# Kernel optimization log

Hardware: AMD Instinct MI355X
Metric: run time of the kernel (lower is better)

## Reference

```python
import jax, jax.numpy as jnp
import numpy as np

N_NODES = 50000
D_MODEL = 128
N_EDGES = 600000
HIDDEN = 128
EDGE_FEAT = 2 * D_MODEL + 2  # 258


def setup_inputs() -> dict:
    key = jax.random.key(0)
    k = jax.random.split(key, 8)
    H = jax.random.normal(k[0], (N_NODES, D_MODEL), dtype=jnp.float32)
    edge_index = jax.random.randint(k[1], (2, N_EDGES), 0, N_NODES, dtype=jnp.int64)
    S_e = jax.random.uniform(k[2], (N_EDGES,), dtype=jnp.float32)
    F_e = jax.random.uniform(k[3], (N_EDGES,), dtype=jnp.float32)
    W1 = jax.random.normal(k[4], (EDGE_FEAT, HIDDEN), dtype=jnp.float32) * (1.0 / np.sqrt(EDGE_FEAT))
    b1 = jnp.zeros((HIDDEN,), dtype=jnp.float32)
    W2 = jax.random.normal(k[5], (HIDDEN, 1), dtype=jnp.float32) * (1.0 / np.sqrt(HIDDEN))
    b2 = jnp.zeros((1,), dtype=jnp.float32)
    return {"H": H, "edge_index": edge_index, "S_e": S_e, "F_e": F_e,
            "W1": W1, "b1": b1, "W2": W2, "b2": b2}


def reference(H, edge_index, S_e, F_e, W1, b1, W2, b2):
    # Gather endpoint node features: [E, D]
    H_u = H[edge_index[0]]
    H_v = H[edge_index[1]]
    H_diff = jnp.abs(H_u - H_v)
    H_prod = H_u * H_v
    # [E, 2D+2]
    edge_features = jnp.concatenate(
        [H_diff, H_prod, S_e[:, None], F_e[:, None]], axis=1)
    # 2-layer MLP with SiLU (dropout is identity in eval mode)
    h = jax.nn.silu(edge_features @ W1 + b1)
    a_e = (h @ W2 + b2)[:, 0]  # [E]
    return a_e
```

## Files before the change

kernel.cpp:

```cpp
#include <hip/hip_runtime.h>


typedef _Float16       half8   __attribute__((ext_vector_type(8)));
typedef _Float16       half4v  __attribute__((ext_vector_type(4)));
typedef unsigned short ushort8 __attribute__((ext_vector_type(8)));
typedef float          f32x4   __attribute__((ext_vector_type(4)));

#define NSEG    8

__device__ __forceinline__ float silu_f(float x) {
    return x / (1.0f + __expf(-x));
}


__global__ __launch_bounds__(256)
void cvt_h_kernel(const float* __restrict__ H, _Float16* __restrict__ Hh, int n4) {
    int i = blockIdx.x * blockDim.x + threadIdx.x;
    if (i < n4) {
        const float4 f = ((const float4*)H)[i];
        half4v h;
        h[0] = (_Float16)f.x; h[1] = (_Float16)f.y;
        h[2] = (_Float16)f.z; h[3] = (_Float16)f.w;
        ((half4v*)Hh)[i] = h;
    }
}

__device__ __forceinline__ void canon(int u, int v, int& a, int& b) {
    const int sw = (u ^ v) & 1;
    a = sw ? v : u;
    b = sw ? u : v;
}

__global__ __launch_bounds__(256)
void hist_kernel(const int* __restrict__ eidx, int* __restrict__ hist,
                 int E, int ASZ, int BBINS) {
    int e = blockIdx.x * blockDim.x + threadIdx.x;
    if (e < E) {
        int a, b;
        canon(eidx[e], eidx[E + e], a, b);
        atomicAdd(&hist[(a / ASZ) * BBINS + (b >> 3)], 1);
    }
}

__global__ __launch_bounds__(256)
void scan1_kernel(int* __restrict__ hist, int* __restrict__ bsum, int NB) {
    __shared__ int s[256];
    const int t = threadIdx.x;
    const int i = blockIdx.x * 256 + t;
    const int v = (i < NB) ? hist[i] : 0;
    s[t] = v;
    __syncthreads();
    for (int off = 1; off < 256; off <<= 1) {
        const int x = (t >= off) ? s[t - off] : 0;
        __syncthreads();
        s[t] += x;
        __syncthreads();
    }
    if (i < NB) hist[i] = s[t] - v;
    if (t == 255) bsum[blockIdx.x] = s[255];
}

__global__ __launch_bounds__(256)
void scan2_kernel(int* __restrict__ bsum, int nb1) {
    __shared__ int s[256];
    const int t = threadIdx.x;
    const int v = (t < nb1) ? bsum[t] : 0;
    s[t] = v;
    __syncthreads();
    for (int off = 1; off < 256; off <<= 1) {
        const int x = (t >= off) ? s[t - off] : 0;
        __syncthreads();
        s[t] += x;
        __syncthreads();
    }
    if (t < nb1) bsum[t] = s[t] - v;
}

__global__ __launch_bounds__(256)
void scan3_kernel(int* __restrict__ hist, const int* __restrict__ bsum, int NB) {
    const int i = blockIdx.x * 256 + threadIdx.x;
    if (i < NB) hist[i] += bsum[blockIdx.x];
}

__global__ __launch_bounds__(64)
void segb_kernel(const int* __restrict__ hist, int* __restrict__ vbs,
                 int BBINS, int E) {
    const int t = threadIdx.x;
    if (t < NSEG) vbs[t] = hist[t * BBINS];
    else if (t == NSEG) vbs[NSEG] = E;
}

__global__ __launch_bounds__(256)
void scatter_kernel(const int* __restrict__ eidx, const float* __restrict__ Se,
                    const float* __restrict__ Fe, int* __restrict__ ofs,
                    int4* __restrict__ recs, int E, int ASZ, int BBINS) {
    int e = blockIdx.x * blockDim.x + threadIdx.x;
    if (e < E) {
        int a, b;
        canon(eidx[e], eidx[E + e], a, b);
        const int key = (a / ASZ) * BBINS + (b >> 3);
        const int pos = atomicAdd(&ofs[key], 1);
        _Float16 sh = (_Float16)Se[e];
        _Float16 fh = (_Float16)Fe[e];
        unsigned pk = (unsigned)*(unsigned short*)&sh
                    | ((unsigned)*(unsigned short*)&fh << 16);
        recs[pos] = make_int4(a, b, e, (int)pk);
    }
}


__device__ __forceinline__ void stage_w1(const float* __restrict__ W1,
                                         _Float16* __restrict__ w1t, int tid) {
    const int n = tid & 127;
    const int g = tid >> 7;
    #pragma unroll
    for (int i = 0; i < 8; ++i) {
        const int kb = g + (i << 2);
        half8 tmp;
        #pragma unroll
        for (int j = 0; j < 8; ++j) {
            const int kp = (kb << 3) + j;
            const int c  = kp >> 5;
            const int r5 = kp & 31;
            const int qq = r5 >> 3;
            const int jj = r5 & 7;
            const int d  = ((c >> 1) << 5) + (qq << 3) + ((c & 1) << 2) + (jj >> 1);
            const int src = ((jj & 1) << 7) + d;
            tmp[j] = (_Float16)W1[src * 128 + n];
        }
        *(half8*)&w1t[n * 256 + ((kb ^ (n & 7)) << 3)] = tmp;
    }
}


__global__ __launch_bounds__(512, 4)
void edgegate_seg(const _Float16* __restrict__ Hh,
                  const int4*  __restrict__ recs,
                  const int*   __restrict__ vbs,
                  int*         __restrict__ ctr,
                  const float* __restrict__ W1,
                  const float* __restrict__ b1,
                  const float* __restrict__ W2,
                  const float* __restrict__ b2,
                  float*       __restrict__ out)
{
    __shared__ _Float16 w1t[128 * 256];
    __shared__ int tkt[2];
    const int tid = threadIdx.x;
    stage_w1(W1, w1t, tid);

    int xcd;
    asm volatile("s_getreg_b32 %0, hwreg(HW_REG_XCC_ID)" : "=s"(xcd));
    xcd &= (NSEG - 1);

    __syncthreads();

    const int lane = tid & 63;
    const int wave = tid >> 6;
    const int q    = lane >> 4;
    const int cb   = lane & 15;
    const int swz  = cb & 7;

    int p = 0;
    for (int sidx = 0; sidx < NSEG; ++sidx) {
        const int seg = (xcd + sidx) & (NSEG - 1);
        const int vs  = vbs[seg];
        const int ve  = vbs[seg + 1];
        const int ner = ve - vs;
        if (ner <= 0) continue;
        const int Tt = (ner + 127) >> 7;

        while (true) {
            if (tid == 0) tkt[p] = atomicAdd(&ctr[seg], 1);
            __syncthreads();
            const int t0 = tkt[p];
            p ^= 1;
            if (t0 >= Tt) break;

            const int ebase = vs + (t0 << 7) + (wave << 4);
            const int e = min(ebase + cb, ve - 1);
            const int4 r = recs[e];
            const int a = r.x, b = r.y, oe = r.z;
            const unsigned pk = (unsigned)r.w;
            const unsigned short sl = (unsigned short)(pk & 0xFFFF);
            const unsigned short fl = (unsigned short)(pk >> 16);
            const float Sf = (float)*(const _Float16*)&sl;
            const float Ff = (float)*(const _Float16*)&fl;

            const _Float16* up = Hh + (size_t)a * 128;
            const _Float16* vp = Hh + (size_t)b * 128;

            f32x4 acc[8];
            #pragma unroll
            for (int t = 0; t < 8; ++t) acc[t] = (f32x4){0.f, 0.f, 0.f, 0.f};

            #pragma unroll
            for (int c8 = 0; c8 < 4; ++c8) {
                const half8 u8 = *(const half8*)(up + (c8 << 5) + (q << 3));
                const half8 v8 = *(const half8*)(vp + (c8 << 5) + (q << 3));
                half8 d8 = u8 - v8;
                ushort8 du = *(ushort8*)&d8;
                du = du & (unsigned short)0x7FFF;
                const half8 da = *(half8*)&du;
                const half8 p8 = u8 * v8;

                half8 ae, ao;
                ae[0]=da[0]; ae[1]=p8[0]; ae[2]=da[1]; ae[3]=p8[1];
                ae[4]=da[2]; ae[5]=p8[2]; ae[6]=da[3]; ae[7]=p8[3];
                ao[0]=da[4]; ao[1]=p8[4]; ao[2]=da[5]; ao[3]=p8[5];
                ao[4]=da[6]; ao[5]=p8[6]; ao[6]=da[7]; ao[7]=p8[7];

                const int kb0 = (((c8 << 1) + 0) * 4 + q) ^ swz;
                const int kb1 = (((c8 << 1) + 1) * 4 + q) ^ swz;
                #pragma unroll
                for (int t = 0; t < 8; ++t) {
                    const half8 b0 = *(const half8*)&w1t[((t << 4) + cb) * 256 + (kb0 << 3)];
                    acc[t] = __builtin_amdgcn_mfma_f32_16x16x32_f16(ae, b0, acc[t], 0, 0, 0);
                }
                #pragma unroll
                for (int t = 0; t < 8; ++t) {
                    const half8 b1f = *(const half8*)&w1t[((t << 4) + cb) * 256 + (kb1 << 3)];
                    acc[t] = __builtin_amdgcn_mfma_f32_16x16x32_f16(ao, b1f, acc[t], 0, 0, 0);
                }
            }

            float s_r[4], f_r[4]; int oe_r[4];
            #pragma unroll
            for (int rr = 0; rr < 4; ++rr) {
                const int src = (q << 2) + rr;
                s_r[rr]  = __shfl(Sf, src);
                f_r[rr]  = __shfl(Ff, src);
                oe_r[rr] = __shfl(oe, src);
            }

            float rs[4] = {0.f, 0.f, 0.f, 0.f};
            #pragma unroll
            for (int t = 0; t < 8; ++t) {
                const int col    = (t << 4) + cb;
                const float w256 = W1[32768 + col];
                const float w257 = W1[32896 + col];
                const float b1c  = b1[col];
                const float w2c  = W2[col];
                const f32x4 av = acc[t];
                #pragma unroll
                for (int rr = 0; rr < 4; ++rr)
                    rs[rr] += silu_f(av[rr] + s_r[rr] * w256 + f_r[rr] * w257 + b1c) * w2c;
            }

            #pragma unroll
            for (int off = 1; off < 16; off <<= 1) {
                #pragma unroll
                for (int rr = 0; rr < 4; ++rr) rs[rr] += __shfl_xor(rs[rr], off);
            }

            if (cb == 0) {
                const float b2v = b2[0];
                #pragma unroll
                for (int rr = 0; rr < 4; ++rr) {
                    const int pe = ebase + (q << 2) + rr;
                    if (pe < ve) out[oe_r[rr]] = rs[rr] + b2v;
                }
            }
        }
    }
}


template<bool F16>
__global__ __launch_bounds__(512, 4)
void edgegate_kernel(const float* __restrict__ H,
                     const _Float16* __restrict__ Hh,
                     const int*   __restrict__ eidx,
                     const float* __restrict__ Se,
                     const float* __restrict__ Fe,
                     const float* __restrict__ W1,
                     const float* __restrict__ b1,
                     const float* __restrict__ W2,
                     const float* __restrict__ b2,
                     float*       __restrict__ out,
                     int E, int ntiles)
{
    __shared__ _Float16 w1t[128 * 256];
    const int tid = threadIdx.x;
    stage_w1(W1, w1t, tid);
    __syncthreads();

    const int lane = tid & 63;
    const int wave = tid >> 6;
    const int q    = lane >> 4;
    const int cb   = lane & 15;
    const int swz  = cb & 7;

    for (int tile = blockIdx.x; tile < ntiles; tile += gridDim.x) {
        const int ebase = tile * 128 + wave * 16;
        int e = ebase + cb;
        if (e >= E) e = E - 1;
        const int u = eidx[e];
        const int v = eidx[E + e];

        f32x4 acc[8];
        #pragma unroll
        for (int t = 0; t < 8; ++t) acc[t] = (f32x4){0.f, 0.f, 0.f, 0.f};

        #pragma unroll
        for (int c8 = 0; c8 < 4; ++c8) {
            half8 ae, ao;
            if constexpr (F16) {
                const _Float16* up = Hh + (size_t)u * 128;
                const _Float16* vp = Hh + (size_t)v * 128;
                const half8 u8 = *(const half8*)(up + (c8 << 5) + (q << 3));
                const half8 v8 = *(const half8*)(vp + (c8 << 5) + (q << 3));
                half8 d8 = u8 - v8;
                ushort8 du = *(ushort8*)&d8;
                du = du & (unsigned short)0x7FFF;
                const half8 da = *(half8*)&du;
                const half8 p8 = u8 * v8;
                ae[0]=da[0]; ae[1]=p8[0]; ae[2]=da[1]; ae[3]=p8[1];
                ae[4]=da[2]; ae[5]=p8[2]; ae[6]=da[3]; ae[7]=p8[3];
                ao[0]=da[4]; ao[1]=p8[4]; ao[2]=da[5]; ao[3]=p8[5];
                ao[4]=da[6]; ao[5]=p8[6]; ao[6]=da[7]; ao[7]=p8[7];
            } else {
                const float* up = H + (size_t)u * 128;
                const float* vp = H + (size_t)v * 128;
                const float4 uu0 = *(const float4*)(up + (c8 << 5) + (q << 3));
                const float4 vv0 = *(const float4*)(vp + (c8 << 5) + (q << 3));
                const float4 uu1 = *(const float4*)(up + (c8 << 5) + (q << 3) + 4);
                const float4 vv1 = *(const float4*)(vp + (c8 << 5) + (q << 3) + 4);
                ae[0]=(_Float16)fabsf(uu0.x-vv0.x); ae[1]=(_Float16)(uu0.x*vv0.x);
                ae[2]=(_Float16)fabsf(uu0.y-vv0.y); ae[3]=(_Float16)(uu0.y*vv0.y);
                ae[4]=(_Float16)fabsf(uu0.z-vv0.z); ae[5]=(_Float16)(uu0.z*vv0.z);
                ae[6]=(_Float16)fabsf(uu0.w-vv0.w); ae[7]=(_Float16)(uu0.w*vv0.w);
                ao[0]=(_Float16)fabsf(uu1.x-vv1.x); ao[1]=(_Float16)(uu1.x*vv1.x);
                ao[2]=(_Float16)fabsf(uu1.y-vv1.y); ao[3]=(_Float16)(uu1.y*vv1.y);
                ao[4]=(_Float16)fabsf(uu1.z-vv1.z); ao[5]=(_Float16)(uu1.z*vv1.z);
                ao[6]=(_Float16)fabsf(uu1.w-vv1.w); ao[7]=(_Float16)(uu1.w*vv1.w);
            }
            const int kb0 = (((c8 << 1) + 0) * 4 + q) ^ swz;
            const int kb1 = (((c8 << 1) + 1) * 4 + q) ^ swz;
            #pragma unroll
            for (int t = 0; t < 8; ++t) {
                const half8 b0 = *(const half8*)&w1t[((t << 4) + cb) * 256 + (kb0 << 3)];
                acc[t] = __builtin_amdgcn_mfma_f32_16x16x32_f16(ae, b0, acc[t], 0, 0, 0);
            }
            #pragma unroll
            for (int t = 0; t < 8; ++t) {
                const half8 b1f = *(const half8*)&w1t[((t << 4) + cb) * 256 + (kb1 << 3)];
                acc[t] = __builtin_amdgcn_mfma_f32_16x16x32_f16(ao, b1f, acc[t], 0, 0, 0);
            }
        }

        const int e0  = ebase + (q << 2);
        const int e0c = (e0 + 3 < E) ? e0 : (E - 4);
        const float4 s4 = *(const float4*)(Se + e0c);
        const float4 f4 = *(const float4*)(Fe + e0c);

        float rs0 = 0.f, rs1 = 0.f, rs2 = 0.f, rs3 = 0.f;
        #pragma unroll
        for (int t = 0; t < 8; ++t) {
            const int col    = (t << 4) + cb;
            const float w256 = W1[32768 + col];
            const float w257 = W1[32896 + col];
            const float b1c  = b1[col];
            const float w2c  = W2[col];
            const f32x4 av = acc[t];
            rs0 += silu_f(av[0] + s4.x * w256 + f4.x * w257 + b1c) * w2c;
            rs1 += silu_f(av[1] + s4.y * w256 + f4.y * w257 + b1c) * w2c;
            rs2 += silu_f(av[2] + s4.z * w256 + f4.z * w257 + b1c) * w2c;
            rs3 += silu_f(av[3] + s4.w * w256 + f4.w * w257 + b1c) * w2c;
        }
        #pragma unroll
        for (int off = 1; off < 16; off <<= 1) {
            rs0 += __shfl_xor(rs0, off);
            rs1 += __shfl_xor(rs1, off);
            rs2 += __shfl_xor(rs2, off);
            rs3 += __shfl_xor(rs3, off);
        }
        if (cb == 0 && e0 < E) {
            const float b2v = b2[0];
            out[e0]     = rs0 + b2v;
            out[e0 + 1] = rs1 + b2v;
            out[e0 + 2] = rs2 + b2v;
            out[e0 + 3] = rs3 + b2v;
        }
    }
}


static inline size_t align256(size_t x) { return (x + 255) & ~(size_t)255; }

extern "C" void kernel_launch(void* const* d_in, const int* in_sizes, int n_in,
                              void* d_out, int out_size, void* d_ws, size_t ws_size,
                              hipStream_t stream)
{
    const float* H    = (const float*)d_in[0];
    const int*   eidx = (const int*)  d_in[1];
    const float* Se   = (const float*)d_in[2];
    const float* Fe   = (const float*)d_in[3];
    const float* W1   = (const float*)d_in[4];
    const float* b1   = (const float*)d_in[5];
    const float* W2   = (const float*)d_in[6];
    const float* b2   = (const float*)d_in[7];
    float* out = (float*)d_out;

    const int nH     = in_sizes[0];
    const int nNodes = nH / 128;
    const int E      = in_sizes[2];
    const int ntiles = (E + 127) / 128;

    const int ASZ   = (nNodes + NSEG - 1) / NSEG;
    const int BBINS = (nNodes + 7) >> 3;
    const int NB    = NSEG * BBINS;
    const int nb1   = (NB + 255) / 256;

    const size_t hhB    = (size_t)nH * sizeof(_Float16);
    const size_t off_g  = align256(hhB);
    const size_t off_bs = align256(off_g + (size_t)(NB + 8) * 4);
    const size_t off_vb = align256(off_bs + 256 * 4);
    const size_t off_r  = align256(off_vb + 16 * 4);
    const size_t need   = off_r + (size_t)E * sizeof(int4);

    if (ws_size >= need && nb1 <= 256) {
        _Float16* Hh   = (_Float16*)((char*)d_ws);
        int*      hist = (int*)     ((char*)d_ws + off_g);
        int*      ctr  = hist + NB;
        int*      bsum = (int*)     ((char*)d_ws + off_bs);
        int*      vbs  = (int*)     ((char*)d_ws + off_vb);
        int4*     recs = (int4*)    ((char*)d_ws + off_r);

        const int n4 = nH / 4;
        hipLaunchKernelGGL(cvt_h_kernel, dim3((n4 + 255) / 256), dim3(256), 0, stream,
                           H, Hh, n4);
        hipMemsetAsync(hist, 0, (size_t)(NB + 8) * 4, stream);
        hipLaunchKernelGGL(hist_kernel, dim3((E + 255) / 256), dim3(256), 0, stream,
                           eidx, hist, E, ASZ, BBINS);
        hipLaunchKernelGGL(scan1_kernel, dim3(nb1), dim3(256), 0, stream,
                           hist, bsum, NB);
        hipLaunchKernelGGL(scan2_kernel, dim3(1), dim3(256), 0, stream, bsum, nb1);
        hipLaunchKernelGGL(scan3_kernel, dim3(nb1), dim3(256), 0, stream,
                           hist, bsum, NB);
        hipLaunchKernelGGL(segb_kernel, dim3(1), dim3(64), 0, stream,
                           hist, vbs, BBINS, E);
        hipLaunchKernelGGL(scatter_kernel, dim3((E + 255) / 256), dim3(256), 0, stream,
                           eidx, Se, Fe, hist, recs, E, ASZ, BBINS);

        hipLaunchKernelGGL(edgegate_seg, dim3(512), dim3(512), 0, stream,
                           Hh, recs, vbs, ctr, W1, b1, W2, b2, out);
    } else if (ws_size >= hhB) {
        _Float16* Hh = (_Float16*)d_ws;
        const int n4 = nH / 4;
        const int grid = (512 < ntiles) ? 512 : ntiles;
        hipLaunchKernelGGL(cvt_h_kernel, dim3((n4 + 255) / 256), dim3(256), 0, stream,
                           H, Hh, n4);
        hipLaunchKernelGGL((edgegate_kernel<true>), dim3(grid), dim3(512), 0, stream,
                           H, Hh, eidx, Se, Fe, W1, b1, W2, b2, out, E, ntiles);
    } else {
        const int grid = (512 < ntiles) ? 512 : ntiles;
        hipLaunchKernelGGL((edgegate_kernel<false>), dim3(grid), dim3(512), 0, stream,
                           H, (const _Float16*)nullptr, eidx, Se, Fe, W1, b1, W2, b2,
                           out, E, ntiles);
    }
}
```

Before: 295.9 us.

## Use 16 node segments, 256-edge tickets, hoist epilogue weights, fuse small setup kernels

Node-range segmentation for sorting edges goes from 8 to 16 segments with 16-node b-bins. Each ticket now covers 256 edges, processed as two 128-edge halves, which halves the atomic ticket grabs and block barriers. The per-column epilogue weights (W1 rows 256/257, b1, W2, b2) are loaded into registers once per block instead of once per tile. The memset is folded into the fp16 conversion kernel and segb into scan3, which removes two launches. The costs are more registers per thread and coarser load balancing across segments.

```diff
diff --git a/kernel.cpp b/kernel.cpp
--- a/kernel.cpp
+++ b/kernel.cpp
@@ -6,7 +6,7 @@
 typedef unsigned short ushort8 __attribute__((ext_vector_type(8)));
 typedef float          f32x4   __attribute__((ext_vector_type(4)));
 
-#define NSEG    8
+#define NSEG2   16
 
 __device__ __forceinline__ float silu_f(float x) {
     return x / (1.0f + __expf(-x));
@@ -14,8 +14,10 @@
 
 
 __global__ __launch_bounds__(256)
-void cvt_h_kernel(const float* __restrict__ H, _Float16* __restrict__ Hh, int n4) {
+void cvt_zero_kernel(const float* __restrict__ H, _Float16* __restrict__ Hh,
+                     int n4, int* __restrict__ zp, int nz) {
     int i = blockIdx.x * blockDim.x + threadIdx.x;
+    if (i < nz) zp[i] = 0;
     if (i < n4) {
         const float4 f = ((const float4*)H)[i];
         half4v h;
@@ -38,7 +40,7 @@
     if (e < E) {
         int a, b;
         canon(eidx[e], eidx[E + e], a, b);
-        atomicAdd(&hist[(a / ASZ) * BBINS + (b >> 3)], 1);
+        atomicAdd(&hist[(a / ASZ) * BBINS + (b >> 4)], 1);
     }
 }
 
@@ -77,17 +79,15 @@
 }
 
 __global__ __launch_bounds__(256)
-void scan3_kernel(int* __restrict__ hist, const int* __restrict__ bsum, int NB) {
+void scan3_kernel(int* __restrict__ hist, const int* __restrict__ bsum,
+                  int* __restrict__ vbs, int NB, int BBINS, int E) {
     const int i = blockIdx.x * 256 + threadIdx.x;
-    if (i < NB) hist[i] += bsum[blockIdx.x];
-}
-
-__global__ __launch_bounds__(64)
-void segb_kernel(const int* __restrict__ hist, int* __restrict__ vbs,
-                 int BBINS, int E) {
-    const int t = threadIdx.x;
-    if (t < NSEG) vbs[t] = hist[t * BBINS];
-    else if (t == NSEG) vbs[NSEG] = E;
+    if (i < NB) {
+        const int val = hist[i] + bsum[blockIdx.x];
+        hist[i] = val;
+        if (i % BBINS == 0) vbs[i / BBINS] = val;
+    }
+    if (i == 0) vbs[NSEG2] = E;
 }
 
 __global__ __launch_bounds__(256)
@@ -98,7 +98,7 @@
     if (e < E) {
         int a, b;
         canon(eidx[e], eidx[E + e], a, b);
-        const int key = (a / ASZ) * BBINS + (b >> 3);
+        const int key = (a / ASZ) * BBINS + (b >> 4);
         const int pos = atomicAdd(&ofs[key], 1);
         _Float16 sh = (_Float16)Se[e];
         _Float16 fh = (_Float16)Fe[e];
@@ -151,9 +151,7 @@
 
     int xcd;
     asm volatile("s_getreg_b32 %0, hwreg(HW_REG_XCC_ID)" : "=s"(xcd));
-    xcd &= (NSEG - 1);
-
-    __syncthreads();
+    xcd &= 7;
 
     const int lane = tid & 63;
     const int wave = tid >> 6;
@@ -161,14 +159,27 @@
     const int cb   = lane & 15;
     const int swz  = cb & 7;
 
+    float w256p[8], w257p[8], b1p[8], w2p[8];
+    #pragma unroll
+    for (int t = 0; t < 8; ++t) {
+        const int col = (t << 4) + cb;
+        w256p[t] = W1[32768 + col];
+        w257p[t] = W1[32896 + col];
+        b1p[t]   = b1[col];
+        w2p[t]   = W2[col];
+    }
+    const float b2v = b2[0];
+
+    __syncthreads();
+
     int p = 0;
-    for (int sidx = 0; sidx < NSEG; ++sidx) {
-        const int seg = (xcd + sidx) & (NSEG - 1);
+    for (int sidx = 0; sidx < NSEG2; ++sidx) {
+        const int seg = ((xcd << 1) + sidx) & (NSEG2 - 1);
         const int vs  = vbs[seg];
         const int ve  = vbs[seg + 1];
         const int ner = ve - vs;
         if (ner <= 0) continue;
-        const int Tt = (ner + 127) >> 7;
+        const int Tt = (ner + 255) >> 8;
 
         while (true) {
             if (tid == 0) tkt[p] = atomicAdd(&ctr[seg], 1);
@@ -177,108 +188,111 @@
             p ^= 1;
             if (t0 >= Tt) break;
 
-            const int ebase = vs + (t0 << 7) + (wave << 4);
-            const int e = min(ebase + cb, ve - 1);
-            const int4 r = recs[e];
-            const int a = r.x, b = r.y, oe = r.z;
-            const unsigned pk = (unsigned)r.w;
-            const unsigned short sl = (unsigned short)(pk & 0xFFFF);
-            const unsigned short fl = (unsigned short)(pk >> 16);
-            const float Sf = (float)*(const _Float16*)&sl;
-            const float Ff = (float)*(const _Float16*)&fl;
-
-            const _Float16* up = Hh + (size_t)a * 128;
-            const _Float16* vp = Hh + (size_t)b * 128;
-
-            f32x4 acc[8];
+            const int base0 = vs + (t0 << 8) + (wave << 4);
+
+            int4 rr2[2];
             #pragma unroll
-            for (int t = 0; t < 8; ++t) acc[t] = (f32x4){0.f, 0.f, 0.f, 0.f};
+            for (int g = 0; g < 2; ++g)
+                rr2[g] = recs[min(base0 + (g << 7) + cb, ve - 1)];
 
             #pragma unroll
-            for (int c8 = 0; c8 < 4; ++c8) {
-                const half8 u8 = *(const half8*)(up + (c8 << 5) + (q << 3));
-                const half8 v8 = *(const half8*)(vp + (c8 << 5) + (q << 3));
-                half8 d8 = u8 - v8;
-                ushort8 du = *(ushort8*)&d8;
-                du = du & (unsigned short)0x7FFF;
-                const half8 da = *(half8*)&du;
-                const half8 p8 = u8 * v8;
-
-                half8 ae, ao;
-                ae[0]=da[0]; ae[1]=p8[0]; ae[2]=da[1]; ae[3]=p8[1];
-                ae[4]=da[2]; ae[5]=p8[2]; ae[6]=da[3]; ae[7]=p8[3];
-                ao[0]=da[4]; ao[1]=p8[4]; ao[2]=da[5]; ao[3]=p8[5];
-                ao[4]=da[6]; ao[5]=p8[6]; ao[6]=da[7]; ao[7]=p8[7];
-
-                const int kb0 = (((c8 << 1) + 0) * 4 + q) ^ swz;
-                const int kb1 = (((c8 << 1) + 1) * 4 + q) ^ swz;
+            for (int g = 0; g < 2; ++g) {
+                const int ebase = base0 + (g << 7);
+                const int4 r = rr2[g];
+                const int a = r.x, b = r.y, oe = r.z;
+                const unsigned pk = (unsigned)r.w;
+                const unsigned short sl = (unsigned short)(pk & 0xFFFF);
+                const unsigned short fl = (unsigned short)(pk >> 16);
+                const float Sf = (float)*(const _Float16*)&sl;
+                const float Ff = (float)*(const _Float16*)&fl;
+
+                const _Float16* up = Hh + (size_t)a * 128;
+                const _Float16* vp = Hh + (size_t)b * 128;
+
+                f32x4 acc[8];
+                #pragma unroll
+                for (int t = 0; t < 8; ++t) acc[t] = (f32x4){0.f, 0.f, 0.f, 0.f};
+
+                #pragma unroll
+                for (int c8 = 0; c8 < 4; ++c8) {
+                    const half8 u8 = *(const half8*)(up + (c8 << 5) + (q << 3));
+                    const half8 v8 = *(const half8*)(vp + (c8 << 5) + (q << 3));
+                    half8 d8 = u8 - v8;
+                    ushort8 du = *(ushort8*)&d8;
+                    du = du & (unsigned short)0x7FFF;
+                    const half8 da = *(half8*)&du;
+                    const half8 p8 = u8 * v8;
+
+                    half8 ae, ao;
+                    ae[0]=da[0]; ae[1]=p8[0]; ae[2]=da[1]; ae[3]=p8[1];
+                    ae[4]=da[2]; ae[5]=p8[2]; ae[6]=da[3]; ae[7]=p8[3];
+                    ao[0]=da[4]; ao[1]=p8[4]; ao[2]=da[5]; ao[3]=p8[5];
+                    ao[4]=da[6]; ao[5]=p8[6]; ao[6]=da[7]; ao[7]=p8[7];
+
+                    const int kb0 = (((c8 << 1) + 0) * 4 + q) ^ swz;
+                    const int kb1 = (((c8 << 1) + 1) * 4 + q) ^ swz;
+                    #pragma unroll
+                    for (int t = 0; t < 8; ++t) {
+                        const half8 b0 = *(const half8*)&w1t[((t << 4) + cb) * 256 + (kb0 << 3)];
+                        acc[t] = __builtin_amdgcn_mfma_f32_16x16x32_f16(ae, b0, acc[t], 0, 0, 0);
+                    }
+                    #pragma unroll
+                    for (int t = 0; t < 8; ++t) {
+                        const half8 b1f = *(const half8*)&w1t[((t << 4) + cb) * 256 + (kb1 << 3)];
+                        acc[t] = __builtin_amdgcn_mfma_f32_16x16x32_f16(ao, b1f, acc[t], 0, 0, 0);
+                    }
+                }
+
+                float s_r[4], f_r[4]; int oe_r[4];
+                #pragma unroll
+                for (int rr = 0; rr < 4; ++rr) {
+                    const int src = (q << 2) + rr;
+                    s_r[rr]  = __shfl(Sf, src);
+                    f_r[rr]  = __shfl(Ff, src);
+                    oe_r[rr] = __shfl(oe, src);
+                }
+
+                float rs[4] = {0.f, 0.f, 0.f, 0.f};
                 #pragma unroll
                 for (int t = 0; t < 8; ++t) {
-                    const half8 b0 = *(const half8*)&w1t[((t << 4) + cb) * 256 + (kb0 << 3)];
-                    acc[t] = __builtin_amdgcn_mfma_f32_16x16x32_f16(ae, b0, acc[t], 0, 0, 0);
+                    const f32x4 av = acc[t];
+                    #pragma unroll
+                    for (int rr = 0; rr < 4; ++rr)
+                        rs[rr] += silu_f(av[rr] + s_r[rr] * w256p[t]
+                                         + f_r[rr] * w257p[t] + b1p[t]) * w2p[t];
                 }
+
                 #pragma unroll
-                for (int t = 0; t < 8; ++t) {
-                    const half8 b1f = *(const half8*)&w1t[((t << 4) + cb) * 256 + (kb1 << 3)];
-                    acc[t] = __builtin_amdgcn_mfma_f32_16x16x32_f16(ao, b1f, acc[t], 0, 0, 0);
+                for (int off = 1; off < 16; off <<= 1) {
+                    #pragma unroll
+                    for (int rr = 0; rr < 4; ++rr) rs[rr] += __shfl_xor(rs[rr], off);
+                }
+
+                if (cb == 0) {
+                    #pragma unroll
+                    for (int rr = 0; rr < 4; ++rr) {
+                        const int pe = ebase + (q << 2) + rr;
+                        if (pe < ve) out[oe_r[rr]] = rs[rr] + b2v;
+                    }
                 }
             }
-
-            float s_r[4], f_r[4]; int oe_r[4];
-            #pragma unroll
-            for (int rr = 0; rr < 4; ++rr) {
-                const int src = (q << 2) + rr;
-                s_r[rr]  = __shfl(Sf, src);
-                f_r[rr]  = __shfl(Ff, src);
-                oe_r[rr] = __shfl(oe, src);
-            }
-
-            float rs[4] = {0.f, 0.f, 0.f, 0.f};
-            #pragma unroll
-            for (int t = 0; t < 8; ++t) {
-                const int col    = (t << 4) + cb;
-                const float w256 = W1[32768 + col];
-                const float w257 = W1[32896 + col];
-                const float b1c  = b1[col];
-                const float w2c  = W2[col];
-                const f32x4 av = acc[t];
-                #pragma unroll
-                for (int rr = 0; rr < 4; ++rr)
-                    rs[rr] += silu_f(av[rr] + s_r[rr] * w256 + f_r[rr] * w257 + b1c) * w2c;
-            }
-
-            #pragma unroll
-            for (int off = 1; off < 16; off <<= 1) {
-                #pragma unroll
-                for (int rr = 0; rr < 4; ++rr) rs[rr] += __shfl_xor(rs[rr], off);
-            }
-
-            if (cb == 0) {
-                const float b2v = b2[0];
-                #pragma unroll
-                for (int rr = 0; rr < 4; ++rr) {
-                    const int pe = ebase + (q << 2) + rr;
-                    if (pe < ve) out[oe_r[rr]] = rs[rr] + b2v;
-                }
-            }
-        }
-    }
-}
-
-
-template<bool F16>
+        }
+    }
+}
+
+
 __global__ __launch_bounds__(512, 4)
-void edgegate_kernel(const float* __restrict__ H,
-                     const _Float16* __restrict__ Hh,
-                     const int*   __restrict__ eidx,
-                     const float* __restrict__ Se,
-                     const float* __restrict__ Fe,
-                     const float* __restrict__ W1,
-                     const float* __restrict__ b1,
-                     const float* __restrict__ W2,
-                     const float* __restrict__ b2,
-                     float*       __restrict__ out,
-                     int E, int ntiles)
+void edgegate_fb(const float* __restrict__ H,
+                 const _Float16* __restrict__ Hh,
+                 const int*   __restrict__ eidx,
+                 const float* __restrict__ Se,
+                 const float* __restrict__ Fe,
+                 const float* __restrict__ W1,
+                 const float* __restrict__ b1,
+                 const float* __restrict__ W2,
+                 const float* __restrict__ b2,
+                 float*       __restrict__ out,
+                 int E, int ntiles, int useF16)
 {
     __shared__ _Float16 w1t[128 * 256];
     const int tid = threadIdx.x;
@@ -305,7 +319,7 @@
         #pragma unroll
         for (int c8 = 0; c8 < 4; ++c8) {
             half8 ae, ao;
-            if constexpr (F16) {
+            if (useF16) {
                 const _Float16* up = Hh + (size_t)u * 128;
                 const _Float16* vp = Hh + (size_t)v * 128;
                 const half8 u8 = *(const half8*)(up + (c8 << 5) + (q << 3));
@@ -407,16 +421,16 @@
     const int E      = in_sizes[2];
     const int ntiles = (E + 127) / 128;
 
-    const int ASZ   = (nNodes + NSEG - 1) / NSEG;
-    const int BBINS = (nNodes + 7) >> 3;
-    const int NB    = NSEG * BBINS;
+    const int ASZ   = (nNodes + NSEG2 - 1) / NSEG2;
+    const int BBINS = (nNodes + 15) >> 4;
+    const int NB    = NSEG2 * BBINS;
     const int nb1   = (NB + 255) / 256;
 
     const size_t hhB    = (size_t)nH * sizeof(_Float16);
     const size_t off_g  = align256(hhB);
-    const size_t off_bs = align256(off_g + (size_t)(NB + 8) * 4);
+    const size_t off_bs = align256(off_g + (size_t)(NB + 16) * 4);
     const size_t off_vb = align256(off_bs + 256 * 4);
-    const size_t off_r  = align256(off_vb + 16 * 4);
+    const size_t off_r  = align256(off_vb + 32 * 4);
     const size_t need   = off_r + (size_t)E * sizeof(int4);
 
     if (ws_size >= need && nb1 <= 256) {
@@ -428,18 +442,15 @@
         int4*     recs = (int4*)    ((char*)d_ws + off_r);
 
         const int n4 = nH / 4;
-        hipLaunchKernelGGL(cvt_h_kernel, dim3((n4 + 255) / 256), dim3(256), 0, stream,
-                           H, Hh, n4);
-        hipMemsetAsync(hist, 0, (size_t)(NB + 8) * 4, stream);
+        hipLaunchKernelGGL(cvt_zero_kernel, dim3((n4 + 255) / 256), dim3(256), 0,
+                           stream, H, Hh, n4, hist, NB + 16);
         hipLaunchKernelGGL(hist_kernel, dim3((E + 255) / 256), dim3(256), 0, stream,
                            eidx, hist, E, ASZ, BBINS);
         hipLaunchKernelGGL(scan1_kernel, dim3(nb1), dim3(256), 0, stream,
                            hist, bsum, NB);
         hipLaunchKernelGGL(scan2_kernel, dim3(1), dim3(256), 0, stream, bsum, nb1);
         hipLaunchKernelGGL(scan3_kernel, dim3(nb1), dim3(256), 0, stream,
-                           hist, bsum, NB);
-        hipLaunchKernelGGL(segb_kernel, dim3(1), dim3(64), 0, stream,
-                           hist, vbs, BBINS, E);
+                           hist, bsum, vbs, NB, BBINS, E);
         hipLaunchKernelGGL(scatter_kernel, dim3((E + 255) / 256), dim3(256), 0, stream,
                            eidx, Se, Fe, hist, recs, E, ASZ, BBINS);
 
@@ -449,14 +460,14 @@
         _Float16* Hh = (_Float16*)d_ws;
         const int n4 = nH / 4;
         const int grid = (512 < ntiles) ? 512 : ntiles;
-        hipLaunchKernelGGL(cvt_h_kernel, dim3((n4 + 255) / 256), dim3(256), 0, stream,
-                           H, Hh, n4);
-        hipLaunchKernelGGL((edgegate_kernel<true>), dim3(grid), dim3(512), 0, stream,
-                           H, Hh, eidx, Se, Fe, W1, b1, W2, b2, out, E, ntiles);
+        hipLaunchKernelGGL(cvt_zero_kernel, dim3((n4 + 255) / 256), dim3(256), 0,
+                           stream, H, Hh, n4, (int*)nullptr, 0);
+        hipLaunchKernelGGL(edgegate_fb, dim3(grid), dim3(512), 0, stream,
+                           H, Hh, eidx, Se, Fe, W1, b1, W2, b2, out, E, ntiles, 1);
     } else {
         const int grid = (512 < ntiles) ? 512 : ntiles;
-        hipLaunchKernelGGL((edgegate_kernel<false>), dim3(grid), dim3(512), 0, stream,
+        hipLaunchKernelGGL(edgegate_fb, dim3(grid), dim3(512), 0, stream,
                            H, (const _Float16*)nullptr, eidx, Se, Fe, W1, b1, W2, b2,
-                           out, E, ntiles);
-    }
-}
+                           out, E, ntiles, 0);
+    }
+}
```

New measurement: 321.5 us. 8.6% more time.

## Fold memset and segment-bound kernels into neighbors; double edge-tile block size

Applied to the files above, without the earlier changes.

Fuses the histogram zeroing into the fp16 conversion kernel and the segment-boundary extraction into scan3, dropping a memset and a tiny kernel launch from the preprocessing chain. The main segmented kernel now runs 1024-thread blocks that process 256 edges per ticket instead of 128, which halves the atomic ticket traffic and amortizes W1 staging over more waves. The fallback kernel's template parameter becomes a runtime flag to reduce code size. The larger blocks may cut occupancy, since 1024 threads with 64KB of LDS may limit residency per CU.

```diff
diff --git a/kernel.cpp b/kernel.cpp
--- a/kernel.cpp
+++ b/kernel.cpp
@@ -14,8 +14,10 @@
 
 
 __global__ __launch_bounds__(256)
-void cvt_h_kernel(const float* __restrict__ H, _Float16* __restrict__ Hh, int n4) {
+void cvt_zero_kernel(const float* __restrict__ H, _Float16* __restrict__ Hh,
+                     int n4, int* __restrict__ zp, int nz) {
     int i = blockIdx.x * blockDim.x + threadIdx.x;
+    if (i < nz) zp[i] = 0;
     if (i < n4) {
         const float4 f = ((const float4*)H)[i];
         half4v h;
@@ -77,17 +79,15 @@
 }
 
 __global__ __launch_bounds__(256)
-void scan3_kernel(int* __restrict__ hist, const int* __restrict__ bsum, int NB) {
+void scan3_kernel(int* __restrict__ hist, const int* __restrict__ bsum,
+                  int* __restrict__ vbs, int NB, int BBINS, int E) {
     const int i = blockIdx.x * 256 + threadIdx.x;
-    if (i < NB) hist[i] += bsum[blockIdx.x];
-}
-
-__global__ __launch_bounds__(64)
-void segb_kernel(const int* __restrict__ hist, int* __restrict__ vbs,
-                 int BBINS, int E) {
-    const int t = threadIdx.x;
-    if (t < NSEG) vbs[t] = hist[t * BBINS];
-    else if (t == NSEG) vbs[NSEG] = E;
+    if (i < NB) {
+        const int val = hist[i] + bsum[blockIdx.x];
+        hist[i] = val;
+        if (i % BBINS == 0) vbs[i / BBINS] = val;
+    }
+    if (i == 0) vbs[NSEG] = E;
 }
 
 __global__ __launch_bounds__(256)
@@ -109,13 +109,15 @@
 }
 
 
+template<int NT>
 __device__ __forceinline__ void stage_w1(const float* __restrict__ W1,
                                          _Float16* __restrict__ w1t, int tid) {
     const int n = tid & 127;
     const int g = tid >> 7;
+    constexpr int GS = NT / 128;
     #pragma unroll
-    for (int i = 0; i < 8; ++i) {
-        const int kb = g + (i << 2);
+    for (int i = 0; i < 32 / GS; ++i) {
+        const int kb = g + i * GS;
         half8 tmp;
         #pragma unroll
         for (int j = 0; j < 8; ++j) {
@@ -133,7 +135,7 @@
 }
 
 
-__global__ __launch_bounds__(512, 4)
+__global__ __launch_bounds__(1024, 4)
 void edgegate_seg(const _Float16* __restrict__ Hh,
                   const int4*  __restrict__ recs,
                   const int*   __restrict__ vbs,
@@ -147,7 +149,7 @@
     __shared__ _Float16 w1t[128 * 256];
     __shared__ int tkt[2];
     const int tid = threadIdx.x;
-    stage_w1(W1, w1t, tid);
+    stage_w1<1024>(W1, w1t, tid);
 
     int xcd;
     asm volatile("s_getreg_b32 %0, hwreg(HW_REG_XCC_ID)" : "=s"(xcd));
@@ -168,7 +170,7 @@
         const int ve  = vbs[seg + 1];
         const int ner = ve - vs;
         if (ner <= 0) continue;
-        const int Tt = (ner + 127) >> 7;
+        const int Tt = (ner + 255) >> 8;
 
         while (true) {
             if (tid == 0) tkt[p] = atomicAdd(&ctr[seg], 1);
@@ -177,7 +179,7 @@
             p ^= 1;
             if (t0 >= Tt) break;
 
-            const int ebase = vs + (t0 << 7) + (wave << 4);
+            const int ebase = vs + (t0 << 8) + (wave << 4);
             const int e = min(ebase + cb, ve - 1);
             const int4 r = recs[e];
             const int a = r.x, b = r.y, oe = r.z;
@@ -266,23 +268,22 @@
 }
 
 
-template<bool F16>
 __global__ __launch_bounds__(512, 4)
-void edgegate_kernel(const float* __restrict__ H,
-                     const _Float16* __restrict__ Hh,
-                     const int*   __restrict__ eidx,
-                     const float* __restrict__ Se,
-                     const float* __restrict__ Fe,
-                     const float* __restrict__ W1,
-                     const float* __restrict__ b1,
-                     const float* __restrict__ W2,
-                     const float* __restrict__ b2,
-                     float*       __restrict__ out,
-                     int E, int ntiles)
+void edgegate_fb(const float* __restrict__ H,
+                 const _Float16* __restrict__ Hh,
+                 const int*   __restrict__ eidx,
+                 const float* __restrict__ Se,
+                 const float* __restrict__ Fe,
+                 const float* __restrict__ W1,
+                 const float* __restrict__ b1,
+                 const float* __restrict__ W2,
+                 const float* __restrict__ b2,
+                 float*       __restrict__ out,
+                 int E, int ntiles, int useF16)
 {
     __shared__ _Float16 w1t[128 * 256];
     const int tid = threadIdx.x;
-    stage_w1(W1, w1t, tid);
+    stage_w1<512>(W1, w1t, tid);
     __syncthreads();
 
     const int lane = tid & 63;
@@ -305,7 +306,7 @@
         #pragma unroll
         for (int c8 = 0; c8 < 4; ++c8) {
             half8 ae, ao;
-            if constexpr (F16) {
+            if (useF16) {
                 const _Float16* up = Hh + (size_t)u * 128;
                 const _Float16* vp = Hh + (size_t)v * 128;
                 const half8 u8 = *(const half8*)(up + (c8 << 5) + (q << 3));
@@ -428,35 +429,32 @@
         int4*     recs = (int4*)    ((char*)d_ws + off_r);
 
         const int n4 = nH / 4;
-        hipLaunchKernelGGL(cvt_h_kernel, dim3((n4 + 255) / 256), dim3(256), 0, stream,
-                           H, Hh, n4);
-        hipMemsetAsync(hist, 0, (size_t)(NB + 8) * 4, stream);
+        hipLaunchKernelGGL(cvt_zero_kernel, dim3((n4 + 255) / 256), dim3(256), 0,
+                           stream, H, Hh, n4, hist, NB + 8);
         hipLaunchKernelGGL(hist_kernel, dim3((E + 255) / 256), dim3(256), 0, stream,
                            eidx, hist, E, ASZ, BBINS);
         hipLaunchKernelGGL(scan1_kernel, dim3(nb1), dim3(256), 0, stream,
                            hist, bsum, NB);
         hipLaunchKernelGGL(scan2_kernel, dim3(1), dim3(256), 0, stream, bsum, nb1);
         hipLaunchKernelGGL(scan3_kernel, dim3(nb1), dim3(256), 0, stream,
-                           hist, bsum, NB);
-        hipLaunchKernelGGL(segb_kernel, dim3(1), dim3(64), 0, stream,
-                           hist, vbs, BBINS, E);
+                           hist, bsum, vbs, NB, BBINS, E);
         hipLaunchKernelGGL(scatter_kernel, dim3((E + 255) / 256), dim3(256), 0, stream,
                            eidx, Se, Fe, hist, recs, E, ASZ, BBINS);
 
-        hipLaunchKernelGGL(edgegate_seg, dim3(512), dim3(512), 0, stream,
+        hipLaunchKernelGGL(edgegate_seg, dim3(512), dim3(1024), 0, stream,
                            Hh, recs, vbs, ctr, W1, b1, W2, b2, out);
     } else if (ws_size >= hhB) {
         _Float16* Hh = (_Float16*)d_ws;
         const int n4 = nH / 4;
         const int grid = (512 < ntiles) ? 512 : ntiles;
-        hipLaunchKernelGGL(cvt_h_kernel, dim3((n4 + 255) / 256), dim3(256), 0, stream,
-                           H, Hh, n4);
-        hipLaunchKernelGGL((edgegate_kernel<true>), dim3(grid), dim3(512), 0, stream,
-                           H, Hh, eidx, Se, Fe, W1, b1, W2, b2, out, E, ntiles);
+        hipLaunchKernelGGL(cvt_zero_kernel, dim3((n4 + 255) / 256), dim3(256), 0,
+                           stream, H, Hh, n4, (int*)nullptr, 0);
+        hipLaunchKernelGGL(edgegate_fb, dim3(grid), dim3(512), 0, stream,
+                           H, Hh, eidx, Se, Fe, W1, b1, W2, b2, out, E, ntiles, 1);
     } else {
         const int grid = (512 < ntiles) ? 512 : ntiles;
-        hipLaunchKernelGGL((edgegate_kernel<false>), dim3(grid), dim3(512), 0, stream,
+        hipLaunchKernelGGL(edgegate_fb, dim3(grid), dim3(512), 0, stream,
                            H, (const _Float16*)nullptr, eidx, Se, Fe, W1, b1, W2, b2,
-                           out, E, ntiles);
-    }
-}
+                           out, E, ntiles, 0);
+    }
+}
```

Result: slower. 303.5 us (+2.6%).
